# Optimization experiments

Hardware: AMD Instinct MI355X
Metric: run time of the kernel (lower is better)

The kernel has to match this reference:

```python
import jax, jax.numpy as jnp
import numpy as np

N, T, P = 1024, 512, 2
H = 128  # hidden_channels == lstm_input_channels == num_fc_concat == 128


def _lin(k, out_dim, in_dim):
    # torch nn.Linear default init: U(-1/sqrt(in), 1/sqrt(in))
    b = 1.0 / np.sqrt(in_dim)
    return jax.random.uniform(k, (out_dim, in_dim), minval=-b, maxval=b, dtype=jnp.float32)


def setup_inputs() -> dict:
    key = jax.random.key(0)
    ks = jax.random.split(key, 12)
    bnd = lambda k, sh, inn: jax.random.uniform(k, sh, minval=-1.0/np.sqrt(inn), maxval=1.0/np.sqrt(inn), dtype=jnp.float32)
    return {
        "x": jax.random.normal(ks[0], (N, T, P), dtype=jnp.float32),
        "enc1_w": _lin(ks[1], 128, 2),
        "enc1_b": bnd(ks[2], (128,), 2),
        "enc2_w": _lin(ks[3], H, 128),
        "enc2_b": bnd(ks[4], (H,), 128),
        "w_ih": _lin(ks[5], 4 * H, H),   # LSTMCell weight_ih, gate order i,f,g,o; bias=False
        "w_hh": _lin(ks[6], 4 * H, H),
        "dec1_w": _lin(ks[7], H, 2 * H),
        "dec1_b": bnd(ks[8], (H,), 2 * H),
        "dec2_w": _lin(ks[9], 1, H),
        "dec2_b": bnd(ks[10], (1,), H),
    }


def reference(x, enc1_w, enc1_b, enc2_w, enc2_b, w_ih, w_hh, dec1_w, dec1_b, dec2_w, dec2_b):
    n = x.shape[0]
    # Encoder MLP applied to every (n, t) position at once: (N,T,2) -> (N,T,H)
    feat = jax.nn.relu(jnp.einsum('ntp,hp->nth', x, enc1_w) + enc1_b)
    feat = jnp.einsum('nth,oh->nto', feat, enc2_w) + enc2_b
    feat_t = jnp.swapaxes(feat, 0, 1)  # (T,N,H)

    def step(carry, xt):
        h, c = carry
        gates = xt @ w_ih.T + h @ w_hh.T  # (N, 4H)
        i, f, g, o = jnp.split(gates, 4, axis=-1)
        c = jax.nn.sigmoid(f) * c + jax.nn.sigmoid(i) * jnp.tanh(g)
        h = jax.nn.sigmoid(o) * jnp.tanh(c)
        return (h, c), h

    init = (jnp.zeros((n, H), dtype=x.dtype), jnp.zeros((n, H), dtype=x.dtype))
    # Shared LSTMCell weights run forward and backward over time
    _, h_fw = jax.lax.scan(step, init, feat_t)            # (T,N,H)
    _, h_bw_rev = jax.lax.scan(step, init, feat_t[::-1])  # (T,N,H) over reversed time
    h_bw = h_bw_rev[::-1]

    final = jax.nn.relu(jnp.concatenate([h_fw, h_bw], axis=-1))  # (T,N,2H)
    q = jax.nn.relu(jnp.einsum('tnk,hk->tnh', final, dec1_w) + dec1_b)
    q = jnp.einsum('tnh,oh->tno', q, dec2_w) + dec2_b  # (T,N,1)
    return jnp.swapaxes(q[..., 0], 0, 1)  # (N,T)
```

## Files before the change

### kernel.cpp

```cpp
#include <hip/hip_runtime.h>
#include <hip/hip_fp16.h>
#include <stdint.h>


#define TN 512
#define NB 1024

typedef __attribute__((ext_vector_type(8))) _Float16 f16x8;
typedef __attribute__((ext_vector_type(4))) float f32x4;

#define MFMA16(a,b,c) __builtin_amdgcn_mfma_f32_16x16x32_f16(a,b,c,0,0,0)
#define RCP(x) __builtin_amdgcn_rcpf(x)

__device__ __forceinline__ f16x8 cvt_frag(const float* p){
  f32x4 a = *(const f32x4*)p;
  f32x4 b = *(const f32x4*)(p+4);
  f16x8 h;
  h[0]=(_Float16)a[0]; h[1]=(_Float16)a[1]; h[2]=(_Float16)a[2]; h[3]=(_Float16)a[3];
  h[4]=(_Float16)b[0]; h[5]=(_Float16)b[1]; h[6]=(_Float16)b[2]; h[7]=(_Float16)b[3];
  return h;
}

__device__ __forceinline__ unsigned short f2h(float f){
  return __half_as_ushort(__float2half(f));
}

__global__ __launch_bounds__(256) void enc_kernel(
    const float* __restrict__ x,  const float* __restrict__ e1w,
    const float* __restrict__ e1b,const float* __restrict__ e2w,
    const float* __restrict__ e2b,
    unsigned short* __restrict__ featA, unsigned short* __restrict__ featB)
{
  __shared__ float xs[64][2];
  __shared__ unsigned int A32[64][68];
  int tid = threadIdx.x;
  long rowbase = (long)blockIdx.x * 64;
  if (tid < 128){
    int i = tid >> 1, cc = tid & 1;
    long row = rowbase + i;
    int t = (int)(row >> 10), n = (int)(row & 1023);
    xs[i][cc] = x[((size_t)n * TN + t) * 2 + cc];
  }
  int w4 = tid >> 6, lane = tid & 63, lq = lane >> 4, lr = lane & 15;
  f16x8 Bf[2][4];
  float b2v[2];
  #pragma unroll
  for (int nt2 = 0; nt2 < 2; nt2++){
    int col = (w4*2 + nt2)*16 + lr;
    b2v[nt2] = e2b[col];
    #pragma unroll
    for (int ks = 0; ks < 4; ks++)
      Bf[nt2][ks] = cvt_frag(e2w + col*128 + ks*32 + lq*8);
  }
  int q = tid >> 6, dp = tid & 63;
  float w00 = e1w[4*dp], w01 = e1w[4*dp+1], w10 = e1w[4*dp+2], w11 = e1w[4*dp+3];
  float b0 = e1b[2*dp], b1 = e1b[2*dp+1];
  __syncthreads();
  #pragma unroll
  for (int rr = 0; rr < 16; rr++){
    int r = q*16 + rr;
    float x0 = xs[r][0], x1 = xs[r][1];
    float v0 = fmaxf(w00*x0 + w01*x1 + b0, 0.f);
    float v1 = fmaxf(w10*x0 + w11*x1 + b1, 0.f);
    A32[r][dp] = (unsigned int)f2h(v0) | ((unsigned int)f2h(v1) << 16);
  }
  __syncthreads();
  #pragma unroll
  for (int Mt = 0; Mt < 4; Mt++){
    f16x8 ah[4];
    #pragma unroll
    for (int ks = 0; ks < 4; ks++)
      ah[ks] = *(const f16x8*)((const unsigned short*)&A32[Mt*16+lr][0] + ks*32 + lq*8);
    f32x4 acc0 = {0.f,0.f,0.f,0.f}, acc1 = {0.f,0.f,0.f,0.f};
    #pragma unroll
    for (int ks = 0; ks < 4; ks++){
      acc0 = MFMA16(ah[ks], Bf[0][ks], acc0);
      acc1 = MFMA16(ah[ks], Bf[1][ks], acc1);
    }
    #pragma unroll
    for (int r = 0; r < 4; r++){
      size_t row = (size_t)(rowbase + Mt*16 + lq*4 + r);
      unsigned short v0 = f2h(acc0[r] + b2v[0]);
      unsigned short v1 = f2h(acc1[r] + b2v[1]);
      featA[row*128 + (w4*2+0)*16 + lr] = v0;
      featA[row*128 + (w4*2+1)*16 + lr] = v1;
      featB[row*128 + (w4*2+0)*16 + lr] = v0;
      featB[row*128 + (w4*2+1)*16 + lr] = v1;
    }
  }
}

#define LSTM_STEP(P, ACCC, ACCN, PFC, PFN) do { \
    _Pragma("unroll") \
    for (int ks = 0; ks < 4; ks++) PFN[ks] = *(const uint4*)(fpp + ks*32); \
    fpp += dstep; \
    f16x8 ah[4]; \
    _Pragma("unroll") \
    for (int ks = 0; ks < 4; ks++) ah[ks] = *(const f16x8*)&hbS[P][smr][ks*32 + lq*8]; \
    _Pragma("unroll") \
    for (int G = 0; G < 4; G++){ \
      _Pragma("unroll") \
      for (int ks = 0; ks < 4; ks++) ACCC[G] = MFMA16(ah[ks], wg[G][4+ks], ACCC[G]); \
    } \
     \
    _Pragma("unroll") \
    for (int G = 0; G < 4; G++) ACCN[G] = MFMA16(*(const f16x8*)&PFC[0], wg[G][0], zero4); \
    float si0 = RCP(1.f + __expf(-ACCC[0][0])); \
    float si1 = RCP(1.f + __expf(-ACCC[0][1])); \
    _Pragma("unroll") \
    for (int G = 0; G < 4; G++) ACCN[G] = MFMA16(*(const f16x8*)&PFC[1], wg[G][1], ACCN[G]); \
    float sf0 = RCP(1.f + __expf(-ACCC[1][0])); \
    float sf1 = RCP(1.f + __expf(-ACCC[1][1])); \
    _Pragma("unroll") \
    for (int G = 0; G < 4; G++) ACCN[G] = MFMA16(*(const f16x8*)&PFC[2], wg[G][2], ACCN[G]); \
    float tg0 = 1.f - 2.f*RCP(__expf(2.f*ACCC[2][0]) + 1.f); \
    float tg1 = 1.f - 2.f*RCP(__expf(2.f*ACCC[2][1]) + 1.f); \
    float so0 = RCP(1.f + __expf(-ACCC[3][0])); \
    float so1 = RCP(1.f + __expf(-ACCC[3][1])); \
    _Pragma("unroll") \
    for (int G = 0; G < 4; G++) ACCN[G] = MFMA16(*(const f16x8*)&PFC[3], wg[G][3], ACCN[G]); \
    c[0] = sf0*c[0] + si0*tg0; \
    c[1] = sf1*c[1] + si1*tg1; \
    float tc0 = 1.f - 2.f*RCP(__expf(2.f*c[0]) + 1.f); \
    float tc1 = 1.f - 2.f*RCP(__expf(2.f*c[1]) + 1.f); \
    float hv0 = so0*tc0, hv1 = so1*tc1; \
    unsigned short hh0 = f2h(hv0), hh1 = f2h(hv1); \
    hbS[(P)^1][lq*2+0][w*16 + lr] = hh0; \
    hbS[(P)^1][lq*2+1][w*16 + lr] = hh1; \
    op[0]   = (hv0 > 0.f) ? hh0 : (unsigned short)0; \
    op[128] = (hv1 > 0.f) ? hh1 : (unsigned short)0; \
    op += dstep; \
    __syncthreads(); \
  } while(0)

__global__ __launch_bounds__(512, 2) void lstm_kernel(
    unsigned short* bufA, unsigned short* bufB,
    const float* __restrict__ wih, const float* __restrict__ whh)
{
  __shared__ __align__(16) unsigned short hbS[2][8][136];
  int tid = threadIdx.x, b = blockIdx.x;
  int dir = b >> 7, n0 = (b & 127) << 3;
  int w = tid >> 6, lane = tid & 63, lq = lane >> 4, lr = lane & 15;
  unsigned short* buf = dir ? bufB : bufA;

  f16x8 wg[4][8];
  #pragma unroll
  for (int G = 0; G < 4; G++){
    int gate = G*128 + w*16 + lr;
    #pragma unroll
    for (int ks = 0; ks < 8; ks++){
      const float* src = (ks < 4) ? (wih + (size_t)gate*128 + ks*32 + lq*8)
                                  : (whh + (size_t)gate*128 + (ks-4)*32 + lq*8);
      wg[G][ks] = cvt_frag(src);
    }
  }

  for (int i = tid; i < 1088; i += 512) ((unsigned int*)hbS)[i] = 0u;

  int smr = ((lr >> 2) << 1) | (lr & 1);
  float c[2] = {0.f, 0.f};
  const f32x4 zero4 = {0.f, 0.f, 0.f, 0.f};
  int t0 = dir ? (TN-1) : 0;
  long dstep = dir ? -(long)(NB*128) : (long)(NB*128);

  const unsigned short* fpp = buf + ((size_t)t0*NB + n0 + smr)*128 + lq*8;
  uint4 pfA[4], pfB[4];
  #pragma unroll
  for (int ks = 0; ks < 4; ks++) pfB[ks] = *(const uint4*)(fpp + ks*32);
  fpp += dstep;
  #pragma unroll
  for (int ks = 0; ks < 4; ks++) pfA[ks] = *(const uint4*)(fpp + ks*32);
  fpp += dstep;

  f32x4 accA[4], accB[4];
  #pragma unroll
  for (int G = 0; G < 4; G++) accA[G] = MFMA16(*(const f16x8*)&pfB[0], wg[G][0], zero4);
  #pragma unroll
  for (int ks = 1; ks < 4; ks++){
    #pragma unroll
    for (int G = 0; G < 4; G++) accA[G] = MFMA16(*(const f16x8*)&pfB[ks], wg[G][ks], accA[G]);
  }

  unsigned short* op = buf + ((size_t)t0*NB + n0 + lq*2)*128 + (w*16 + lr);
  __syncthreads();

  for (int s2 = 0; s2 < TN/2; s2++){
    LSTM_STEP(0, accA, accB, pfA, pfB);
    LSTM_STEP(1, accB, accA, pfB, pfA);
  }
}

__global__ __launch_bounds__(256) void dec_kernel(
    const unsigned short* __restrict__ hfw, const unsigned short* __restrict__ hbw,
    const float* __restrict__ d1w, const float* __restrict__ d1b,
    const float* __restrict__ d2w, const float* __restrict__ d2b,
    float* __restrict__ out)
{
  __shared__ unsigned short A[64][264];
  __shared__ float partial[4][64];
  int tid = threadIdx.x;
  long rowbase = (long)blockIdx.x * 64;
  #pragma unroll
  for (int u = 0; u < 8; u++){
    int chunk = u*256 + tid;
    int row = chunk >> 5, seg = chunk & 31;
    const unsigned short* src = (seg < 16)
        ? (hfw + ((size_t)(rowbase + row))*128 + seg*8)
        : (hbw + ((size_t)(rowbase + row))*128 + (seg-16)*8);
    *(uint4*)&A[row][seg*8] = *(const uint4*)src;
  }
  int w4 = tid >> 6, lane = tid & 63, lq = lane >> 4, lr = lane & 15;
  f16x8 Bf[2][8];
  float b1v[2], w2v[2];
  #pragma unroll
  for (int nt2 = 0; nt2 < 2; nt2++){
    int col = (w4*2 + nt2)*16 + lr;
    b1v[nt2] = d1b[col];
    w2v[nt2] = d2w[col];
    #pragma unroll
    for (int ks = 0; ks < 8; ks++)
      Bf[nt2][ks] = cvt_frag(d1w + col*256 + ks*32 + lq*8);
  }
  float b2s = d2b[0];
  __syncthreads();
  #pragma unroll
  for (int Mt = 0; Mt < 4; Mt++){
    f16x8 ah[8];
    #pragma unroll
    for (int ks = 0; ks < 8; ks++)
      ah[ks] = *(const f16x8*)&A[Mt*16+lr][ks*32 + lq*8];
    f32x4 acc0 = {0.f,0.f,0.f,0.f}, acc1 = {0.f,0.f,0.f,0.f};
    #pragma unroll
    for (int ks = 0; ks < 8; ks++){
      acc0 = MFMA16(ah[ks], Bf[0][ks], acc0);
      acc1 = MFMA16(ah[ks], Bf[1][ks], acc1);
    }
    #pragma unroll
    for (int r = 0; r < 4; r++){
      float p = fmaxf(acc0[r] + b1v[0], 0.f) * w2v[0]
              + fmaxf(acc1[r] + b1v[1], 0.f) * w2v[1];
      p += __shfl_xor(p, 1);
      p += __shfl_xor(p, 2);
      p += __shfl_xor(p, 4);
      p += __shfl_xor(p, 8);
      if (lr == 0) partial[w4][Mt*16 + lq*4 + r] = p;
    }
  }
  __syncthreads();
  if (tid < 64){
    long row = rowbase + tid;
    int t = (int)(row >> 10), n = (int)(row & 1023);
    out[(size_t)n*TN + t] = partial[0][tid] + partial[1][tid]
                          + partial[2][tid] + partial[3][tid] + b2s;
  }
}

extern "C" void kernel_launch(void* const* d_in, const int* in_sizes, int n_in,
                              void* d_out, int out_size, void* d_ws, size_t ws_size,
                              hipStream_t stream)
{
  const float* x   = (const float*)d_in[0];
  const float* e1w = (const float*)d_in[1];
  const float* e1b = (const float*)d_in[2];
  const float* e2w = (const float*)d_in[3];
  const float* e2b = (const float*)d_in[4];
  const float* wih = (const float*)d_in[5];
  const float* whh = (const float*)d_in[6];
  const float* d1w = (const float*)d_in[7];
  const float* d1b = (const float*)d_in[8];
  const float* d2w = (const float*)d_in[9];
  const float* d2b = (const float*)d_in[10];
  float* out = (float*)d_out;

  if (ws_size < ((size_t)256 << 20)) return;

  char* ws = (char*)d_ws;
  unsigned short* bufA = (unsigned short*)ws;
  unsigned short* bufB = (unsigned short*)(ws + (((size_t)128) << 20));

  hipLaunchKernelGGL(enc_kernel, dim3(8192), dim3(256), 0, stream, x, e1w, e1b, e2w, e2b, bufA, bufB);
  hipLaunchKernelGGL(lstm_kernel, dim3(256), dim3(512), 0, stream, bufA, bufB, wih, whh);
  hipLaunchKernelGGL(dec_kernel, dim3(8192), dim3(256), 0, stream, bufA, bufB, d1w, d1b, d2w, d2b, out);
}
```

Baseline: 677.0 us.

## Split LSTM gates across two wave groups with LDS exchange per step

Doubles the LSTM block to 1024 threads. Each wave now computes two of the four gates, so the recurrent h@Whh MFMA chain per wave is halved. Group 1 writes its g/o pre-activations to shared memory, and group 0 computes the cell update and h. The input projection for the next step is issued in whichever group is idle in each half-step. The cost is a second __syncthreads per step, plus the LDS round trip and divergence between the two groups on the serial critical path.

```diff
diff --git a/kernel.cpp b/kernel.cpp
--- a/kernel.cpp
+++ b/kernel.cpp
@@ -90,103 +90,128 @@
   }
 }
 
-#define LSTM_STEP(P, ACCC, ACCN, PFC, PFN) do { \
-    _Pragma("unroll") \
-    for (int ks = 0; ks < 4; ks++) PFN[ks] = *(const uint4*)(fpp + ks*32); \
-    fpp += dstep; \
+#define LSTM_STEP(P, ACCC, ACCN) do { \
     f16x8 ah[4]; \
     _Pragma("unroll") \
     for (int ks = 0; ks < 4; ks++) ah[ks] = *(const f16x8*)&hbS[P][smr][ks*32 + lq*8]; \
     _Pragma("unroll") \
-    for (int G = 0; G < 4; G++){ \
+    for (int ks = 0; ks < 4; ks++){ \
+      ACCC[0] = MFMA16(ah[ks], wg[0][4+ks], ACCC[0]); \
+      ACCC[1] = MFMA16(ah[ks], wg[1][4+ks], ACCC[1]); \
+    } \
+    if (gp == 0){ \
+      ACCN[0] = MFMA16(*(const f16x8*)&pf[0], wg[0][0], zero4); \
+      ACCN[1] = MFMA16(*(const f16x8*)&pf[0], wg[1][0], zero4); \
       _Pragma("unroll") \
-      for (int ks = 0; ks < 4; ks++) ACCC[G] = MFMA16(ah[ks], wg[G][4+ks], ACCC[G]); \
+      for (int ks = 1; ks < 4; ks++){ \
+        ACCN[0] = MFMA16(*(const f16x8*)&pf[ks], wg[0][ks], ACCN[0]); \
+        ACCN[1] = MFMA16(*(const f16x8*)&pf[ks], wg[1][ks], ACCN[1]); \
+      } \
+      _Pragma("unroll") \
+      for (int ks = 0; ks < 4; ks++) pf[ks] = *(const uint4*)(fpp + ks*32); \
+      fpp += dstep; \
+    } else { \
+      gw[d][0][lane] = ACCC[0][0]; \
+      gw[d][1][lane] = ACCC[1][0]; \
+      gw[d][2][lane] = ACCC[0][1]; \
+      gw[d][3][lane] = ACCC[1][1]; \
     } \
-     \
-    _Pragma("unroll") \
-    for (int G = 0; G < 4; G++) ACCN[G] = MFMA16(*(const f16x8*)&PFC[0], wg[G][0], zero4); \
-    float si0 = RCP(1.f + __expf(-ACCC[0][0])); \
-    float si1 = RCP(1.f + __expf(-ACCC[0][1])); \
-    _Pragma("unroll") \
-    for (int G = 0; G < 4; G++) ACCN[G] = MFMA16(*(const f16x8*)&PFC[1], wg[G][1], ACCN[G]); \
-    float sf0 = RCP(1.f + __expf(-ACCC[1][0])); \
-    float sf1 = RCP(1.f + __expf(-ACCC[1][1])); \
-    _Pragma("unroll") \
-    for (int G = 0; G < 4; G++) ACCN[G] = MFMA16(*(const f16x8*)&PFC[2], wg[G][2], ACCN[G]); \
-    float tg0 = 1.f - 2.f*RCP(__expf(2.f*ACCC[2][0]) + 1.f); \
-    float tg1 = 1.f - 2.f*RCP(__expf(2.f*ACCC[2][1]) + 1.f); \
-    float so0 = RCP(1.f + __expf(-ACCC[3][0])); \
-    float so1 = RCP(1.f + __expf(-ACCC[3][1])); \
-    _Pragma("unroll") \
-    for (int G = 0; G < 4; G++) ACCN[G] = MFMA16(*(const f16x8*)&PFC[3], wg[G][3], ACCN[G]); \
-    c[0] = sf0*c[0] + si0*tg0; \
-    c[1] = sf1*c[1] + si1*tg1; \
-    float tc0 = 1.f - 2.f*RCP(__expf(2.f*c[0]) + 1.f); \
-    float tc1 = 1.f - 2.f*RCP(__expf(2.f*c[1]) + 1.f); \
-    float hv0 = so0*tc0, hv1 = so1*tc1; \
-    unsigned short hh0 = f2h(hv0), hh1 = f2h(hv1); \
-    hbS[(P)^1][lq*2+0][w*16 + lr] = hh0; \
-    hbS[(P)^1][lq*2+1][w*16 + lr] = hh1; \
-    op[0]   = (hv0 > 0.f) ? hh0 : (unsigned short)0; \
-    op[128] = (hv1 > 0.f) ? hh1 : (unsigned short)0; \
-    op += dstep; \
-    __syncthreads(); \
+    __syncthreads();    \
+    if (gp == 0){ \
+      float gv0 = gw[d][0][lane], ov0 = gw[d][1][lane]; \
+      float gv1 = gw[d][2][lane], ov1 = gw[d][3][lane]; \
+      float iv0 = ACCC[0][0], fv0 = ACCC[1][0]; \
+      float iv1 = ACCC[0][1], fv1 = ACCC[1][1]; \
+      float si0 = RCP(1.f + __expf(-iv0)); \
+      float sf0 = RCP(1.f + __expf(-fv0)); \
+      float so0 = RCP(1.f + __expf(-ov0)); \
+      float tg0 = 1.f - 2.f*RCP(__expf(2.f*gv0) + 1.f); \
+      float si1 = RCP(1.f + __expf(-iv1)); \
+      float sf1 = RCP(1.f + __expf(-fv1)); \
+      float so1 = RCP(1.f + __expf(-ov1)); \
+      float tg1 = 1.f - 2.f*RCP(__expf(2.f*gv1) + 1.f); \
+      c[0] = sf0*c[0] + si0*tg0; \
+      c[1] = sf1*c[1] + si1*tg1; \
+      float tc0 = 1.f - 2.f*RCP(__expf(2.f*c[0]) + 1.f); \
+      float tc1 = 1.f - 2.f*RCP(__expf(2.f*c[1]) + 1.f); \
+      float hv0 = so0*tc0, hv1 = so1*tc1; \
+      unsigned short hh0 = f2h(hv0), hh1 = f2h(hv1); \
+      hbS[(P)^1][lq*2+0][d*16 + lr] = hh0; \
+      hbS[(P)^1][lq*2+1][d*16 + lr] = hh1; \
+      op[0]   = (hv0 > 0.f) ? hh0 : (unsigned short)0; \
+      op[128] = (hv1 > 0.f) ? hh1 : (unsigned short)0; \
+      op += dstep; \
+    } else { \
+      ACCN[0] = MFMA16(*(const f16x8*)&pf[0], wg[0][0], zero4); \
+      ACCN[1] = MFMA16(*(const f16x8*)&pf[0], wg[1][0], zero4); \
+      _Pragma("unroll") \
+      for (int ks = 1; ks < 4; ks++){ \
+        ACCN[0] = MFMA16(*(const f16x8*)&pf[ks], wg[0][ks], ACCN[0]); \
+        ACCN[1] = MFMA16(*(const f16x8*)&pf[ks], wg[1][ks], ACCN[1]); \
+      } \
+      _Pragma("unroll") \
+      for (int ks = 0; ks < 4; ks++) pf[ks] = *(const uint4*)(fpp + ks*32); \
+      fpp += dstep; \
+    } \
+    __syncthreads();    \
   } while(0)
 
-__global__ __launch_bounds__(512, 2) void lstm_kernel(
+__global__ __launch_bounds__(1024, 4) void lstm_kernel(
     unsigned short* bufA, unsigned short* bufB,
     const float* __restrict__ wih, const float* __restrict__ whh)
 {
-  __shared__ __align__(16) unsigned short hbS[2][8][136];
+  __shared__ __align__(16) unsigned short hbS[2][8][132];
+  __shared__ float gw[8][4][65];
   int tid = threadIdx.x, b = blockIdx.x;
   int dir = b >> 7, n0 = (b & 127) << 3;
   int w = tid >> 6, lane = tid & 63, lq = lane >> 4, lr = lane & 15;
+  int d = w & 7, gp = w >> 3;
   unsigned short* buf = dir ? bufB : bufA;
-
-  f16x8 wg[4][8];
-  #pragma unroll
-  for (int G = 0; G < 4; G++){
-    int gate = G*128 + w*16 + lr;
+  long dstep = dir ? -(long)(NB*128) : (long)(NB*128);
+  long t0 = dir ? (TN-1) : 0;
+  const f32x4 zero4 = {0.f, 0.f, 0.f, 0.f};
+
+  f16x8 wg[2][8];
+  #pragma unroll
+  for (int G2 = 0; G2 < 2; G2++){
+    int gate = (gp*2 + G2)*128 + d*16 + lr;
     #pragma unroll
     for (int ks = 0; ks < 8; ks++){
       const float* src = (ks < 4) ? (wih + (size_t)gate*128 + ks*32 + lq*8)
                                   : (whh + (size_t)gate*128 + (ks-4)*32 + lq*8);
-      wg[G][ks] = cvt_frag(src);
-    }
-  }
-
-  for (int i = tid; i < 1088; i += 512) ((unsigned int*)hbS)[i] = 0u;
+      wg[G2][ks] = cvt_frag(src);
+    }
+  }
+
+  for (int i = tid; i < 1056; i += 1024) ((unsigned int*)hbS)[i] = 0u;
 
   int smr = ((lr >> 2) << 1) | (lr & 1);
   float c[2] = {0.f, 0.f};
-  const f32x4 zero4 = {0.f, 0.f, 0.f, 0.f};
-  int t0 = dir ? (TN-1) : 0;
-  long dstep = dir ? -(long)(NB*128) : (long)(NB*128);
 
   const unsigned short* fpp = buf + ((size_t)t0*NB + n0 + smr)*128 + lq*8;
-  uint4 pfA[4], pfB[4];
-  #pragma unroll
-  for (int ks = 0; ks < 4; ks++) pfB[ks] = *(const uint4*)(fpp + ks*32);
+  uint4 f0[4], pf[4];
+  #pragma unroll
+  for (int ks = 0; ks < 4; ks++) f0[ks] = *(const uint4*)(fpp + ks*32);
   fpp += dstep;
   #pragma unroll
-  for (int ks = 0; ks < 4; ks++) pfA[ks] = *(const uint4*)(fpp + ks*32);
+  for (int ks = 0; ks < 4; ks++) pf[ks] = *(const uint4*)(fpp + ks*32);
   fpp += dstep;
 
-  f32x4 accA[4], accB[4];
-  #pragma unroll
-  for (int G = 0; G < 4; G++) accA[G] = MFMA16(*(const f16x8*)&pfB[0], wg[G][0], zero4);
+  f32x4 accA[2], accB[2];
+  accA[0] = MFMA16(*(const f16x8*)&f0[0], wg[0][0], zero4);
+  accA[1] = MFMA16(*(const f16x8*)&f0[0], wg[1][0], zero4);
   #pragma unroll
   for (int ks = 1; ks < 4; ks++){
-    #pragma unroll
-    for (int G = 0; G < 4; G++) accA[G] = MFMA16(*(const f16x8*)&pfB[ks], wg[G][ks], accA[G]);
-  }
-
-  unsigned short* op = buf + ((size_t)t0*NB + n0 + lq*2)*128 + (w*16 + lr);
+    accA[0] = MFMA16(*(const f16x8*)&f0[ks], wg[0][ks], accA[0]);
+    accA[1] = MFMA16(*(const f16x8*)&f0[ks], wg[1][ks], accA[1]);
+  }
+
+  unsigned short* op = buf + ((size_t)t0*NB + n0 + lq*2)*128 + d*16 + lr;
   __syncthreads();
 
   for (int s2 = 0; s2 < TN/2; s2++){
-    LSTM_STEP(0, accA, accB, pfA, pfB);
-    LSTM_STEP(1, accB, accA, pfB, pfA);
+    LSTM_STEP(0, accA, accB);
+    LSTM_STEP(1, accB, accA);
   }
 }
 
@@ -279,6 +304,6 @@
   unsigned short* bufB = (unsigned short*)(ws + (((size_t)128) << 20));
 
   hipLaunchKernelGGL(enc_kernel, dim3(8192), dim3(256), 0, stream, x, e1w, e1b, e2w, e2b, bufA, bufB);
-  hipLaunchKernelGGL(lstm_kernel, dim3(256), dim3(512), 0, stream, bufA, bufB, wih, whh);
+  hipLaunchKernelGGL(lstm_kernel, dim3(256), dim3(1024), 0, stream, bufA, bufB, wih, whh);
   hipLaunchKernelGGL(dec_kernel, dim3(8192), dim3(256), 0, stream, bufA, bufB, d1w, d1b, d2w, d2b, out);
 }
```

Measured after the change: 955.8 us. 41.2% more time.
